# Optimization experiments

Measured on AMD Instinct MI355X. Metric: run time of the kernel, lower is better.

## Reference

```python
import jax, jax.numpy as jnp
import numpy as np
from jax import lax

BATCH = 4096
HID = 512
T = 20


def setup_inputs() -> dict:
    key = jax.random.key(0)
    ks = jax.random.split(key, 12)
    B2 = BATCH * 2
    inp = {
        "x": jax.random.normal(ks[0], (BATCH, 2, T, 2), jnp.float32),
        "x_agents": jax.random.normal(ks[1], (BATCH, 2), jnp.float32),  # unused by forward
        "h0": jax.random.normal(ks[2], (B2, HID), jnp.float32),
        "c0": jax.random.normal(ks[3], (B2, HID), jnp.float32),
        # LSTMCell params (PyTorch layout: gates stacked as [i, f, g, o])
        "W_ih": jax.random.normal(ks[4], (4 * HID, 2), jnp.float32) * 0.05,
        "W_hh": jax.random.normal(ks[5], (4 * HID, HID), jnp.float32) * 0.05,
        "b_ih": jax.random.normal(ks[6], (4 * HID,), jnp.float32) * 0.05,
        "b_hh": jax.random.normal(ks[7], (4 * HID,), jnp.float32) * 0.05,
        # MLP head
        "fc1_w": jax.random.normal(ks[8], (HID, 2 * T * HID), jnp.float32) * 0.01,
        "fc1_b": jax.random.normal(ks[9], (HID,), jnp.float32) * 0.01,
        "fc2_w": jax.random.normal(ks[10], (1, HID), jnp.float32) * 0.05,
        "fc2_b": jax.random.normal(ks[11], (1,), jnp.float32) * 0.05,
        "training_step": 2,
    }
    return inp


def reference(x, x_agents, h0, c0, W_ih, W_hh, b_ih, b_hh, fc1_w, fc1_b, fc2_w, fc2_b, training_step):
    # training_step == 2 path (default) of the original module.
    batch = x.shape[0]
    H = W_hh.shape[1]
    xs = x.reshape(batch * 2, T, 2).transpose(1, 0, 2)  # [T, B2, 2]

    def step(carry, xt):
        h, c = carry
        gates = xt @ W_ih.T + b_ih + h @ W_hh.T + b_hh  # [B2, 4H]
        i, f, g, o = jnp.split(gates, 4, axis=-1)
        i = jax.nn.sigmoid(i)
        f = jax.nn.sigmoid(f)
        g = jnp.tanh(g)
        o = jax.nn.sigmoid(o)
        c_new = f * c + i * g
        h_new = o * jnp.tanh(c_new)
        return (h_new, c_new), h_new

    _, hs = lax.scan(step, (h0, c0), xs)  # hs: [T, B2, H]
    states = hs.transpose(1, 0, 2).reshape(batch, 2 * T * H)  # [batch, 2*T*H]
    out = jax.nn.relu(states @ fc1_w.T + fc1_b) @ fc2_w.T + fc2_b
    return jax.nn.sigmoid(out)
```

## Files before the change

kernel.cpp:

```cpp
#include <hip/hip_runtime.h>
#include <hip/hip_bf16.h>

#define TSTEPS 20
#define SMEM_BYTES 131072

typedef __bf16 bf16x8 __attribute__((ext_vector_type(8)));
typedef float f32x4 __attribute__((ext_vector_type(4)));
typedef _Float16 f16x4 __attribute__((ext_vector_type(4)));
typedef unsigned short u16;

__device__ __forceinline__ u16 f2bf(float f) {
  unsigned u = __builtin_bit_cast(unsigned, f);
  u = (u + 0x7FFFu + ((u >> 16) & 1u)) >> 16;
  return (u16)u;
}
__device__ __forceinline__ float rcp_(float v) { return __builtin_amdgcn_rcpf(v); }
__device__ __forceinline__ float sig_(float v) { return rcp_(1.f + __expf(-v)); }
__device__ __forceinline__ float tanh_(float v) { return 1.f - 2.f * rcp_(1.f + __expf(2.f * v)); }

#define MFMA16(a, b, c) __builtin_amdgcn_mfma_f32_16x16x32_bf16((a), (b), (c), 0, 0, 0)
#define BAR() asm volatile("s_barrier" ::: "memory")
#define WAITV(n) asm volatile("s_waitcnt vmcnt(" #n ")" ::: "memory")
#define WAITLG() asm volatile("s_waitcnt lgkmcnt(0)" ::: "memory")

__device__ __forceinline__ void gload16(const u16* g, u16* lds) {
#if defined(__HIP_DEVICE_COMPILE__)
  __builtin_amdgcn_global_load_lds(
      (const __attribute__((address_space(1))) unsigned*)g,
      (__attribute__((address_space(3))) unsigned*)lds, 16, 0, 0);
#endif
}

__global__ void convert_f32_bf16(const float* __restrict__ s, u16* __restrict__ d, int n) {
  int i = (blockIdx.x * blockDim.x + threadIdx.x) * 4;
  if (i + 3 < n) {
    float4 v = *reinterpret_cast<const float4*>(s + i);
    ushort4 o;
    o.x = f2bf(v.x); o.y = f2bf(v.y); o.z = f2bf(v.z); o.w = f2bf(v.w);
    *reinterpret_cast<ushort4*>(d + i) = o;
  }
}

__global__ void convert_whh_p(const float* __restrict__ w, u16* __restrict__ d) {
  int p = blockIdx.x;
  int k = threadIdx.x;
  int j = p & 15, f = (p >> 4) & 3, wg = (p >> 6) & 3, s = p >> 8;
  int orig = (f << 9) + (s << 6) + (wg << 4) + j;
  d[p * 512 + k] = f2bf(w[orig * 512 + k]);
}

__global__ void bx_prep(const float* __restrict__ Wih, const float* __restrict__ bih,
                        const float* __restrict__ bhh, u16* __restrict__ Bx) {
  int p = blockIdx.x * blockDim.x + threadIdx.x;
  if (p >= 2048) return;
  int j = p & 15, f = (p >> 4) & 3, wg = (p >> 6) & 3, s = p >> 8;
  int o = (f << 9) + (s << 6) + (wg << 4) + j;
  u16* row = Bx + p * 32;
  row[0] = f2bf(Wih[o * 2 + 0]);
  row[1] = f2bf(Wih[o * 2 + 1]);
  row[2] = f2bf(bih[o] + bhh[o]);
#pragma unroll
  for (int k = 3; k < 32; ++k) row[k] = 0;
}

__global__ void init_state(const float* __restrict__ h0, const float* __restrict__ c0,
                           u16* __restrict__ hbf, _Float16* __restrict__ cws,
                           float* __restrict__ facc, int nh, int nacc) {
  int i = blockIdx.x * blockDim.x + threadIdx.x;
  if (i < nh) {
    hbf[i] = f2bf(h0[i]);
    int r = i & 3, mt = (i >> 2) & 7, lane = (i >> 5) & 63, wid = (i >> 11) & 7, bid = i >> 14;
    int s = (bid >> 3) & 7, nb = (bid & 7) * 4 + (bid >> 6);
    int wm = wid >> 2, wn = wid & 3;
    int jl = lane & 15, kg = lane >> 4;
    int n = nb * 256 + wm * 128 + mt * 16 + kg * 4 + r;
    int u = s * 64 + wn * 16 + jl;
    cws[i] = (_Float16)c0[n * 512 + u];
  }
  if (i < nacc) facc[i] = 0.f;
}

__global__ __launch_bounds__(512, 1) void step256(
    const u16* __restrict__ Wp,
    const u16* __restrict__ Bxg,
    const float* __restrict__ x,
    const u16* __restrict__ hin,
    u16* __restrict__ hout,
    _Float16* __restrict__ cws,
    const u16* __restrict__ fc1w,
    float* __restrict__ facc,
    int t, int doLstm, int doFc1) {
  extern __shared__ char S[];

  const int tid = threadIdx.x;
  const int lane = tid & 63, wid = tid >> 6;
  const int jl = lane & 15, kg = lane >> 4;
  const int bid = blockIdx.x;
  const int s = (bid >> 3) & 7;
  const int nb = (bid & 7) * 4 + (bid >> 6);
  const int n0 = nb * 256;
  const int srow = tid >> 3;
  const int sw = (tid & 7) ^ (srow & 7);

  if (doLstm) {
    const int wm = wid >> 2, wn = wid & 3;
    const int u = s * 64 + wn * 16 + jl;
    const int swz0 = (kg ^ (jl & 7)) * 16;
    const int swz1 = ((4 + kg) ^ (jl & 7)) * 16;
    const int aB0 = wm * 16384 + jl * 128 + swz0;
    const int aB1 = wm * 16384 + jl * 128 + swz1;
    const int bB0 = 32768 + wn * 8192 + jl * 128 + swz0;
    const int bB1 = 32768 + wn * 8192 + jl * 128 + swz1;
    const u16* srcA = hin + (n0 + srow) * 512 + sw * 8;
    const u16* srcB = Wp + (s * 256 + srow) * 512 + sw * 8;

    f32x4 acc[8][4];
#pragma unroll
    for (int mt = 0; mt < 8; ++mt)
#pragma unroll
      for (int f = 0; f < 4; ++f) acc[mt][f] = (f32x4){0.f, 0.f, 0.f, 0.f};

    float2 xv = {0.f, 0.f};
    if (tid < 256) xv = *reinterpret_cast<const float2*>(x + (n0 + tid) * 40 + t * 2);
    {
      const int r0 = tid >> 2, ch = tid & 3;
      gload16(Bxg + (s * 256 + 0 * 128 + r0) * 32 + ch * 8, (u16*)(S + 32768 + 0 * 8192 + wid * 1024));
      gload16(Bxg + (s * 256 + 1 * 128 + r0) * 32 + ch * 8, (u16*)(S + 32768 + 1 * 8192 + wid * 1024));
    }
#pragma unroll
    for (int q = 0; q < 4; ++q) {
      gload16(srcA + q * 32768, (u16*)(S + 65536 + q * 8192 + wid * 1024));
      gload16(srcB + q * 32768, (u16*)(S + 65536 + 32768 + q * 8192 + wid * 1024));
    }
    if (tid < 256) {
      u16 row0[8] = {f2bf(xv.x), f2bf(xv.y), 0x3F80u, 0, 0, 0, 0, 0};
      *reinterpret_cast<uint4*>(S + tid * 64) = *reinterpret_cast<const uint4*>(row0);
      uint4 z = {0u, 0u, 0u, 0u};
      *reinterpret_cast<uint4*>(S + tid * 64 + 16) = z;
      *reinterpret_cast<uint4*>(S + tid * 64 + 32) = z;
      *reinterpret_cast<uint4*>(S + tid * 64 + 48) = z;
    }
    WAITLG();
    WAITV(8);
    BAR();
    {
#pragma unroll
      for (int mt = 0; mt < 8; ++mt) {
        bf16x8 a = *reinterpret_cast<const bf16x8*>(S + (wm * 128 + mt * 16 + jl) * 64 + kg * 16);
#pragma unroll
        for (int f = 0; f < 4; ++f) {
          bf16x8 b = *reinterpret_cast<const bf16x8*>(S + 32768 + (wn * 64 + f * 16 + jl) * 64 + kg * 16);
          acc[mt][f] = MFMA16(a, b, acc[mt][f]);
        }
      }
    }
    BAR();

#define LSTAGE(kt, p)                                                              \
  do {                                                                             \
    _Pragma("unroll") for (int q = 0; q < 4; ++q) {                                \
      gload16(srcA + q * 32768 + (kt) * 64, (u16*)(S + (p) * 65536 + q * 8192 + wid * 1024)); \
      gload16(srcB + q * 32768 + (kt) * 64, (u16*)(S + (p) * 65536 + 32768 + q * 8192 + wid * 1024)); \
    }                                                                              \
  } while (0)
#define LCOMP(p)                                                                   \
  do {                                                                             \
    bf16x8 a0[8], b0[4];                                                           \
    _Pragma("unroll") for (int mt = 0; mt < 8; ++mt)                               \
        a0[mt] = *reinterpret_cast<const bf16x8*>(S + (p) * 65536 + aB0 + mt * 2048); \
    _Pragma("unroll") for (int f = 0; f < 4; ++f)                                  \
        b0[f] = *reinterpret_cast<const bf16x8*>(S + (p) * 65536 + bB0 + f * 2048); \
    _Pragma("unroll") for (int mt = 0; mt < 8; ++mt)                               \
      _Pragma("unroll") for (int f = 0; f < 4; ++f)                                \
        acc[mt][f] = MFMA16(a0[mt], b0[f], acc[mt][f]);                            \
    _Pragma("unroll") for (int mt = 0; mt < 8; ++mt)                               \
        a0[mt] = *reinterpret_cast<const bf16x8*>(S + (p) * 65536 + aB1 + mt * 2048); \
    _Pragma("unroll") for (int f = 0; f < 4; ++f)                                  \
        b0[f] = *reinterpret_cast<const bf16x8*>(S + (p) * 65536 + bB1 + f * 2048); \
    _Pragma("unroll") for (int mt = 0; mt < 8; ++mt)                               \
      _Pragma("unroll") for (int f = 0; f < 4; ++f)                                \
        acc[mt][f] = MFMA16(a0[mt], b0[f], acc[mt][f]);                            \
  } while (0)

#pragma unroll
    for (int kt = 0; kt < 8; ++kt) {
      if (kt < 7) {
        if ((kt + 1) & 1) LSTAGE(kt + 1, 0); else LSTAGE(kt + 1, 1);
        WAITV(8);
      } else {
        WAITV(0);
      }
      BAR();
      if (kt & 1) LCOMP(0); else LCOMP(1);
      BAR();
    }

    _Float16* cbase = cws + ((bid * 8 + wid) * 64 + lane) * 32;
#pragma unroll
    for (int mt = 0; mt < 8; ++mt) {
      f16x4 cv = *reinterpret_cast<f16x4*>(cbase + mt * 4);
      f16x4 cn;
      float hn[4];
#pragma unroll
      for (int r = 0; r < 4; ++r) {
        float iv = sig_(acc[mt][0][r]);
        float fv = sig_(acc[mt][1][r]);
        float gv = tanh_(acc[mt][2][r]);
        float ov = sig_(acc[mt][3][r]);
        float c2 = fv * (float)cv[r] + iv * gv;
        cn[r] = (_Float16)c2;
        hn[r] = ov * tanh_(c2);
      }
      *reinterpret_cast<f16x4*>(cbase + mt * 4) = cn;
#pragma unroll
      for (int r = 0; r < 4; ++r)
        hout[(n0 + wm * 128 + mt * 16 + kg * 4 + r) * 512 + u] = f2bf(hn[r]);
    }
  }

  if (doFc1) {
    const int Fm0 = nb * 128, Fj0 = s * 64;
    const int Fwm = wid >> 1, Fwn = wid & 1;
    const int tf = t - 1;

    f32x4 fa[2][2];
#pragma unroll
    for (int a = 0; a < 2; ++a)
#pragma unroll
      for (int b = 0; b < 2; ++b) fa[a][b] = (f32x4){0.f, 0.f, 0.f, 0.f};

#define FSTAGE(kt, p)                                                              \
  do {                                                                             \
    const int an_ = (kt) >> 2, hb_ = ((kt) & 3) * 128;                             \
    _Pragma("unroll") for (int kh = 0; kh < 2; ++kh) {                             \
      _Pragma("unroll") for (int q = 0; q < 2; ++q)                                \
        gload16(hin + (2 * (Fm0 + q * 64 + srow) + an_) * 512 + hb_ + kh * 64 + sw * 8, \
                (u16*)(S + (p) * 65536 + kh * 16384 + q * 8192 + wid * 1024));     \
      gload16(fc1w + (Fj0 + srow) * 20480 + an_ * 10240 + tf * 512 + hb_ + kh * 64 + sw * 8, \
              (u16*)(S + (p) * 65536 + 32768 + kh * 8192 + wid * 1024));           \
    }                                                                              \
  } while (0)
#define FCOMP(p)                                                                   \
  do {                                                                             \
    _Pragma("unroll") for (int kk = 0; kk < 4; ++kk) {                             \
      const int kh_ = kk >> 1;                                                     \
      const int cs_ = (((kk & 1) * 4 + kg) ^ (jl & 7)) * 16;                       \
      bf16x8 af[2], bf[2];                                                         \
      _Pragma("unroll") for (int mf = 0; mf < 2; ++mf)                             \
          af[mf] = *reinterpret_cast<const bf16x8*>(                               \
              S + (p) * 65536 + kh_ * 16384 + (Fwm * 32 + mf * 16 + jl) * 128 + cs_); \
      _Pragma("unroll") for (int jf = 0; jf < 2; ++jf)                             \
          bf[jf] = *reinterpret_cast<const bf16x8*>(                               \
              S + (p) * 65536 + 32768 + kh_ * 8192 + (Fwn * 32 + jf * 16 + jl) * 128 + cs_); \
      _Pragma("unroll") for (int mf = 0; mf < 2; ++mf)                             \
        _Pragma("unroll") for (int jf = 0; jf < 2; ++jf)                           \
          fa[mf][jf] = MFMA16(af[mf], bf[jf], fa[mf][jf]);                         \
    }                                                                              \
  } while (0)

    FSTAGE(0, 1);
#pragma unroll
    for (int kt = 0; kt < 8; ++kt) {
      if (kt < 7) {
        if ((kt + 1) & 1) FSTAGE(kt + 1, 0); else FSTAGE(kt + 1, 1);
        WAITV(6);
      } else {
        WAITV(0);
      }
      BAR();
      if (kt & 1) FCOMP(0); else FCOMP(1);
      BAR();
    }
#pragma unroll
    for (int mf = 0; mf < 2; ++mf)
#pragma unroll
      for (int jf = 0; jf < 2; ++jf) {
        int j = Fj0 + Fwn * 32 + jf * 16 + jl;
#pragma unroll
        for (int r = 0; r < 4; ++r) {
          int m = Fm0 + Fwm * 32 + mf * 16 + kg * 4 + r;
          facc[m * 512 + j] += fa[mf][jf][r];
        }
      }
  }
}

__global__ __launch_bounds__(256) void head_kernel(
    const float* __restrict__ acc, const float* __restrict__ fc1b,
    const float* __restrict__ fc2w, const float* __restrict__ fc2b,
    float* __restrict__ out) {
  int lane = threadIdx.x & 63;
  int row = blockIdx.x * 4 + (threadIdx.x >> 6);
  float sum = 0.f;
#pragma unroll
  for (int j = lane; j < 512; j += 64)
    sum += fmaxf(acc[row * 512 + j] + fc1b[j], 0.f) * fc2w[j];
#pragma unroll
  for (int off = 32; off; off >>= 1) sum += __shfl_down(sum, off);
  if (lane == 0) out[row] = 1.f / (1.f + __expf(-(sum + fc2b[0])));
}

extern "C" void kernel_launch(void* const* d_in, const int* in_sizes, int n_in,
                              void* d_out, int out_size, void* d_ws, size_t ws_size,
                              hipStream_t stream) {
  const float* x = (const float*)d_in[0];
  const float* h0 = (const float*)d_in[2];
  const float* c0 = (const float*)d_in[3];
  const float* Wih = (const float*)d_in[4];
  const float* Whh = (const float*)d_in[5];
  const float* bih = (const float*)d_in[6];
  const float* bhh = (const float*)d_in[7];
  const float* fc1w = (const float*)d_in[8];
  const float* fc1b = (const float*)d_in[9];
  const float* fc2w = (const float*)d_in[10];
  const float* fc2b = (const float*)d_in[11];
  float* out = (float*)d_out;

  char* ws = (char*)d_ws;
  const size_t MB = 1 << 20;
  u16* Wp = (u16*)(ws);
  u16* fc1_bf = (u16*)(ws + 2 * MB);
  u16* hbf0 = (u16*)(ws + 22 * MB);
  u16* hbf1 = (u16*)(ws + 30 * MB);
  _Float16* cws = (_Float16*)(ws + 38 * MB);
  float* facc = (float*)(ws + 46 * MB);
  u16* Bxg = (u16*)(ws + 54 * MB);

  (void)hipFuncSetAttribute(reinterpret_cast<const void*>(step256),
                            hipFuncAttributeMaxDynamicSharedMemorySize, SMEM_BYTES);

  convert_whh_p<<<2048, 512, 0, stream>>>(Whh, Wp);
  bx_prep<<<8, 256, 0, stream>>>(Wih, bih, bhh, Bxg);
  convert_f32_bf16<<<10240, 256, 0, stream>>>(fc1w, fc1_bf, 512 * 20480);
  init_state<<<16384, 256, 0, stream>>>(h0, c0, hbf0, cws, facc, 8192 * 512, 4096 * 512);

  u16* hb[2] = {hbf0, hbf1};
  for (int t = 0; t <= TSTEPS; ++t) {
    step256<<<256, 512, SMEM_BYTES, stream>>>(
        Wp, Bxg, x, hb[t & 1], hb[(t + 1) & 1], cws, fc1_bf, facc,
        t, t < TSTEPS ? 1 : 0, t > 0 ? 1 : 0);
  }
  head_kernel<<<1024, 256, 0, stream>>>(facc, fc1b, fc2w, fc2b, out);
}
```

Baseline: 611.1 us.

## Prefetch fc1 stage during LSTM tail, store fc1 accumulator in fp16, transpose x

Issues the first fc1 tile loads inside the last LSTM k-iteration so they overlap the LSTM compute tail and the cell update. Stores the fc1 partial-sum accumulator as fp16 instead of fp32, halving its read-modify-write traffic on every step. Adds a prep kernel that transposes x so each step's input read is contiguous. The fp16 accumulator over 20 steps loses precision, and the extra prep kernel adds a launch.

```diff
diff --git a/kernel.cpp b/kernel.cpp
--- a/kernel.cpp
+++ b/kernel.cpp
@@ -63,9 +63,17 @@
   for (int k = 3; k < 32; ++k) row[k] = 0;
 }
 
+__global__ void xt_prep(const float* __restrict__ x, float* __restrict__ xt) {
+  int id = blockIdx.x * blockDim.x + threadIdx.x;
+  if (id >= 163840) return;
+  int tt = id >> 13, n = id & 8191;
+  float2 v = *reinterpret_cast<const float2*>(x + n * 40 + tt * 2);
+  *reinterpret_cast<float2*>(xt + tt * 16384 + n * 2) = v;
+}
+
 __global__ void init_state(const float* __restrict__ h0, const float* __restrict__ c0,
                            u16* __restrict__ hbf, _Float16* __restrict__ cws,
-                           float* __restrict__ facc, int nh, int nacc) {
+                           _Float16* __restrict__ facc, int nh, int nacc) {
   int i = blockIdx.x * blockDim.x + threadIdx.x;
   if (i < nh) {
     hbf[i] = f2bf(h0[i]);
@@ -77,18 +85,18 @@
     int u = s * 64 + wn * 16 + jl;
     cws[i] = (_Float16)c0[n * 512 + u];
   }
-  if (i < nacc) facc[i] = 0.f;
+  if (i < nacc) facc[i] = (_Float16)0.f;
 }
 
 __global__ __launch_bounds__(512, 1) void step256(
     const u16* __restrict__ Wp,
     const u16* __restrict__ Bxg,
-    const float* __restrict__ x,
+    const float* __restrict__ xt,
     const u16* __restrict__ hin,
     u16* __restrict__ hout,
     _Float16* __restrict__ cws,
     const u16* __restrict__ fc1w,
-    float* __restrict__ facc,
+    _Float16* __restrict__ facc,
     int t, int doLstm, int doFc1) {
   extern __shared__ char S[];
 
@@ -101,6 +109,21 @@
   const int n0 = nb * 256;
   const int srow = tid >> 3;
   const int sw = (tid & 7) ^ (srow & 7);
+  const int Fm0 = nb * 128, Fj0 = s * 64;
+  const int Fwm = wid >> 1, Fwn = wid & 1;
+  const int tf = t - 1;
+
+#define FSTAGE(kt, p)                                                              \
+  do {                                                                             \
+    const int an_ = (kt) >> 2, hb_ = ((kt) & 3) * 128;                             \
+    _Pragma("unroll") for (int kh = 0; kh < 2; ++kh) {                             \
+      _Pragma("unroll") for (int q = 0; q < 2; ++q)                                \
+        gload16(hin + (2 * (Fm0 + q * 64 + srow) + an_) * 512 + hb_ + kh * 64 + sw * 8, \
+                (u16*)(S + (p) * 65536 + kh * 16384 + q * 8192 + wid * 1024));     \
+      gload16(fc1w + (Fj0 + srow) * 20480 + an_ * 10240 + tf * 512 + hb_ + kh * 64 + sw * 8, \
+              (u16*)(S + (p) * 65536 + 32768 + kh * 8192 + wid * 1024));           \
+    }                                                                              \
+  } while (0)
 
   if (doLstm) {
     const int wm = wid >> 2, wn = wid & 3;
@@ -121,7 +144,7 @@
       for (int f = 0; f < 4; ++f) acc[mt][f] = (f32x4){0.f, 0.f, 0.f, 0.f};
 
     float2 xv = {0.f, 0.f};
-    if (tid < 256) xv = *reinterpret_cast<const float2*>(x + (n0 + tid) * 40 + t * 2);
+    if (tid < 256) xv = *reinterpret_cast<const float2*>(xt + t * 16384 + (n0 + tid) * 2);
     {
       const int r0 = tid >> 2, ch = tid & 3;
       gload16(Bxg + (s * 256 + 0 * 128 + r0) * 32 + ch * 8, (u16*)(S + 32768 + 0 * 8192 + wid * 1024));
@@ -188,7 +211,7 @@
         if ((kt + 1) & 1) LSTAGE(kt + 1, 0); else LSTAGE(kt + 1, 1);
         WAITV(8);
       } else {
-        WAITV(0);
+        if (doFc1) { FSTAGE(0, 1); WAITV(6); } else { WAITV(0); }
       }
       BAR();
       if (kt & 1) LCOMP(0); else LCOMP(1);
@@ -219,27 +242,12 @@
   }
 
   if (doFc1) {
-    const int Fm0 = nb * 128, Fj0 = s * 64;
-    const int Fwm = wid >> 1, Fwn = wid & 1;
-    const int tf = t - 1;
-
     f32x4 fa[2][2];
 #pragma unroll
     for (int a = 0; a < 2; ++a)
 #pragma unroll
       for (int b = 0; b < 2; ++b) fa[a][b] = (f32x4){0.f, 0.f, 0.f, 0.f};
 
-#define FSTAGE(kt, p)                                                              \
-  do {                                                                             \
-    const int an_ = (kt) >> 2, hb_ = ((kt) & 3) * 128;                             \
-    _Pragma("unroll") for (int kh = 0; kh < 2; ++kh) {                             \
-      _Pragma("unroll") for (int q = 0; q < 2; ++q)                                \
-        gload16(hin + (2 * (Fm0 + q * 64 + srow) + an_) * 512 + hb_ + kh * 64 + sw * 8, \
-                (u16*)(S + (p) * 65536 + kh * 16384 + q * 8192 + wid * 1024));     \
-      gload16(fc1w + (Fj0 + srow) * 20480 + an_ * 10240 + tf * 512 + hb_ + kh * 64 + sw * 8, \
-              (u16*)(S + (p) * 65536 + 32768 + kh * 8192 + wid * 1024));           \
-    }                                                                              \
-  } while (0)
 #define FCOMP(p)                                                                   \
   do {                                                                             \
     _Pragma("unroll") for (int kk = 0; kk < 4; ++kk) {                             \
@@ -258,7 +266,7 @@
     }                                                                              \
   } while (0)
 
-    FSTAGE(0, 1);
+    if (!doLstm) FSTAGE(0, 1);
 #pragma unroll
     for (int kt = 0; kt < 8; ++kt) {
       if (kt < 7) {
@@ -279,14 +287,14 @@
 #pragma unroll
         for (int r = 0; r < 4; ++r) {
           int m = Fm0 + Fwm * 32 + mf * 16 + kg * 4 + r;
-          facc[m * 512 + j] += fa[mf][jf][r];
+          facc[m * 512 + j] = (_Float16)((float)facc[m * 512 + j] + fa[mf][jf][r]);
         }
       }
   }
 }
 
 __global__ __launch_bounds__(256) void head_kernel(
-    const float* __restrict__ acc, const float* __restrict__ fc1b,
+    const _Float16* __restrict__ acc, const float* __restrict__ fc1b,
     const float* __restrict__ fc2w, const float* __restrict__ fc2b,
     float* __restrict__ out) {
   int lane = threadIdx.x & 63;
@@ -294,7 +302,7 @@
   float sum = 0.f;
 #pragma unroll
   for (int j = lane; j < 512; j += 64)
-    sum += fmaxf(acc[row * 512 + j] + fc1b[j], 0.f) * fc2w[j];
+    sum += fmaxf((float)acc[row * 512 + j] + fc1b[j], 0.f) * fc2w[j];
 #pragma unroll
   for (int off = 32; off; off >>= 1) sum += __shfl_down(sum, off);
   if (lane == 0) out[row] = 1.f / (1.f + __expf(-(sum + fc2b[0])));
@@ -323,21 +331,23 @@
   u16* hbf0 = (u16*)(ws + 22 * MB);
   u16* hbf1 = (u16*)(ws + 30 * MB);
   _Float16* cws = (_Float16*)(ws + 38 * MB);
-  float* facc = (float*)(ws + 46 * MB);
-  u16* Bxg = (u16*)(ws + 54 * MB);
+  _Float16* facc = (_Float16*)(ws + 46 * MB);
+  u16* Bxg = (u16*)(ws + 50 * MB);
+  float* xt = (float*)(ws + 51 * MB);
 
   (void)hipFuncSetAttribute(reinterpret_cast<const void*>(step256),
                             hipFuncAttributeMaxDynamicSharedMemorySize, SMEM_BYTES);
 
   convert_whh_p<<<2048, 512, 0, stream>>>(Whh, Wp);
   bx_prep<<<8, 256, 0, stream>>>(Wih, bih, bhh, Bxg);
+  xt_prep<<<640, 256, 0, stream>>>(x, xt);
   convert_f32_bf16<<<10240, 256, 0, stream>>>(fc1w, fc1_bf, 512 * 20480);
   init_state<<<16384, 256, 0, stream>>>(h0, c0, hbf0, cws, facc, 8192 * 512, 4096 * 512);
 
   u16* hb[2] = {hbf0, hbf1};
   for (int t = 0; t <= TSTEPS; ++t) {
     step256<<<256, 512, SMEM_BYTES, stream>>>(
-        Wp, Bxg, x, hb[t & 1], hb[(t + 1) & 1], cws, fc1_bf, facc,
+        Wp, Bxg, xt, hb[t & 1], hb[(t + 1) & 1], cws, fc1_bf, facc,
         t, t < TSTEPS ? 1 : 0, t > 0 ? 1 : 0);
   }
   head_kernel<<<1024, 256, 0, stream>>>(facc, fc1b, fc2w, fc2b, out);
```

New measurement: 594.8 us. -2.7%, faster.
